# Optimization experiments

Measured on AMD Instinct MI355X. Metric: run time of the kernel, lower is better.

## Reference

```python
import jax, jax.numpy as jnp
import numpy as np
import math

# ---- config (matches init_kwargs / Mamba defaults) ----
B_SZ = 16
IMG = 224
PATCH = 16
D_MODEL = 384
DEPTH = 24
D_INNER = 2 * D_MODEL          # expand=2
D_STATE = 16
D_CONV = 4
DT_RANK = math.ceil(D_MODEL / D_STATE)
N_CLASSES = 1000
L_TOK = (IMG // PATCH) ** 2     # 196

C_CURV = 0.5
SQRT_C = math.sqrt(C_CURV)
MAX_NORM = 0.95 / SQRT_C

# ---- StablePoincareBall ops ----
def _norm(x):
    return jnp.sqrt(jnp.sum(x * x, axis=-1, keepdims=True) + 1e-15)

def expmap0(u):
    n = jnp.clip(_norm(u), 1e-8, 5.0)
    res = jnp.tanh(SQRT_C * n) / SQRT_C * (u / n)
    rn = _norm(res)
    scale = jnp.where(rn > MAX_NORM, MAX_NORM / rn, jnp.ones_like(rn))
    return res * scale

def logmap0(y):
    n = jnp.clip(_norm(y), 1e-8, MAX_NORM)
    return jnp.arctanh(jnp.minimum(SQRT_C * n, 0.95)) / SQRT_C * (y / n)

def mobius_add(a, b):
    xy = jnp.sum(a * b, -1, keepdims=True)
    x2 = jnp.sum(a * a, -1, keepdims=True)
    y2 = jnp.sum(b * b, -1, keepdims=True)
    num = (1 + 2 * C_CURV * xy + C_CURV * y2) * a + (1 - C_CURV * x2) * b
    den = 1 + 2 * C_CURV * xy + (C_CURV ** 2) * x2 * y2
    return num / jnp.maximum(den, 1e-15)

def mobius_matvec(M, x):
    xn = jnp.maximum(_norm(x), 1e-8)
    mx = x @ M.T
    mxn = jnp.maximum(_norm(mx), 1e-8)
    t = jnp.tanh(mxn / xn * jnp.arctanh(jnp.minimum(SQRT_C * xn, 1.0 - 1e-5)))
    return t * mx / (mxn * SQRT_C)

def hyp_layernorm(x, gamma, beta, eps=1e-5):
    t = logmap0(x)
    mean = t.mean(-1, keepdims=True)
    # torch .std() is unbiased (ddof=1)
    var = jnp.sum((t - mean) ** 2, -1, keepdims=True) / (t.shape[-1] - 1)
    tn = (t - mean) / (jnp.sqrt(var) + eps)
    return expmap0(tn * gamma + beta)

def silu(x):
    return x * jax.nn.sigmoid(x)

# ---- Mamba selective scan (recompute dA per step; carry only h) ----
def selective_scan(u, dt, A, Bm, Cm):
    # u, dt: (B,L,Din); A: (Din,N); Bm, Cm: (B,L,N)
    def step(h, inp):
        dt_t, B_t, C_t, u_t = inp              # (B,Din),(B,N),(B,N),(B,Din)
        dA = jnp.exp(dt_t[..., None] * A)      # (B,Din,N)
        h = dA * h + dt_t[..., None] * B_t[:, None, :] * u_t[..., None]
        y = jnp.sum(h * C_t[:, None, :], -1)   # (B,Din)
        return h, y
    h0 = jnp.zeros((u.shape[0], u.shape[2], A.shape[1]), u.dtype)
    _, ys = jax.lax.scan(step, h0, (dt.transpose(1, 0, 2), Bm.transpose(1, 0, 2),
                                    Cm.transpose(1, 0, 2), u.transpose(1, 0, 2)))
    return ys.transpose(1, 0, 2)               # (B,L,Din)

def mamba_mixer(x, in_w, cw, cb, xp_w, dt_w, dt_b, A_log, Dp, out_w):
    xz = x @ in_w.T                            # (B,L,2*Din)
    xc, z = xz[..., :D_INNER], xz[..., D_INNER:]
    xt = xc.transpose(0, 2, 1)                 # (B,Din,L)
    xpad = jnp.pad(xt, ((0, 0), (0, 0), (D_CONV - 1, 0)))
    L = xt.shape[-1]
    conv = sum(cw[:, k][None, :, None] * xpad[:, :, k:k + L] for k in range(D_CONV))
    conv = conv + cb[None, :, None]
    u = silu(conv.transpose(0, 2, 1))          # (B,L,Din)
    dbl = u @ xp_w.T                           # (B,L,dt_rank+2N)
    dt_r = dbl[..., :DT_RANK]
    Bm = dbl[..., DT_RANK:DT_RANK + D_STATE]
    Cm = dbl[..., DT_RANK + D_STATE:]
    dt = jax.nn.softplus(dt_r @ dt_w.T + dt_b)
    A = -jnp.exp(A_log)
    y = selective_scan(u, dt, A, Bm, Cm) + Dp * u
    y = y * silu(z)
    return y @ out_w.T


def setup_inputs() -> dict:
    key = jax.random.key(0)
    ks = jax.random.split(key, 24)
    f32 = jnp.float32
    inp = {}
    inp['x'] = jax.random.normal(ks[0], (B_SZ, 3, IMG, IMG), f32)
    inp['patch_w'] = jax.random.normal(ks[1], (D_MODEL, 3, PATCH, PATCH), f32) * 0.02
    inp['patch_b'] = jax.random.normal(ks[2], (D_MODEL,), f32) * 0.005
    inp['hyp_w'] = jax.random.normal(ks[3], (D_MODEL, D_MODEL), f32) * (1.0 / math.sqrt(D_MODEL))
    inp['hyp_b'] = jax.random.normal(ks[4], (D_MODEL,), f32) * 0.01
    inp['pe_gamma'] = jnp.ones((D_MODEL,), f32)
    inp['pe_beta'] = jnp.zeros((D_MODEL,), f32)
    inp['pos_embed'] = jax.random.normal(ks[5], (1, L_TOK, D_MODEL), f32) * 0.02
    inp['in_proj_w'] = jax.random.normal(ks[6], (DEPTH, 2 * D_INNER, D_MODEL), f32) * 0.02
    inp['conv_w'] = jax.random.normal(ks[7], (DEPTH, D_INNER, D_CONV), f32) * 0.1
    inp['conv_b'] = jnp.zeros((DEPTH, D_INNER), f32)
    inp['x_proj_w'] = jax.random.normal(ks[8], (DEPTH, DT_RANK + 2 * D_STATE, D_INNER), f32) * 0.02
    inp['dt_proj_w'] = jax.random.normal(ks[9], (DEPTH, D_INNER, DT_RANK), f32) * (1.0 / math.sqrt(DT_RANK))
    inp['dt_proj_b'] = jnp.log(jnp.expm1(jnp.full((DEPTH, D_INNER), 0.01, f32)))  # dt init ~0.01
    inp['A_log'] = jnp.tile(jnp.log(jnp.arange(1, D_STATE + 1, dtype=f32))[None, None, :], (DEPTH, D_INNER, 1))
    inp['Dp'] = jnp.ones((DEPTH, D_INNER), f32)
    inp['out_proj_w'] = jax.random.normal(ks[10], (DEPTH, D_MODEL, D_INNER), f32) * (0.02 / math.sqrt(DEPTH))
    inp['gamma'] = jnp.ones((DEPTH, D_MODEL), f32)
    inp['beta'] = jnp.zeros((DEPTH, D_MODEL), f32)
    inp['gamma_f'] = jnp.ones((D_MODEL,), f32)
    inp['beta_f'] = jnp.zeros((D_MODEL,), f32)
    inp['prototypes'] = expmap0(jax.random.normal(ks[11], (N_CLASSES, D_MODEL), f32) * 0.1)
    return inp


def reference(x, patch_w, patch_b, hyp_w, hyp_b, pe_gamma, pe_beta, pos_embed,
              in_proj_w, conv_w, conv_b, x_proj_w, dt_proj_w, dt_proj_b,
              A_log, Dp, out_proj_w, gamma, beta, gamma_f, beta_f, prototypes):
    # patch embed conv
    feat = jax.lax.conv_general_dilated(x, patch_w, (PATCH, PATCH), 'VALID',
                                        dimension_numbers=('NCHW', 'OIHW', 'NCHW'))
    feat = feat + patch_b[None, :, None, None]
    B, D, Hp, Wp = feat.shape
    tokens = feat.reshape(B, D, Hp * Wp).transpose(0, 2, 1)   # (B,L,D)
    h = expmap0(tokens)
    h = mobius_add(mobius_matvec(hyp_w, h), hyp_b)
    h = hyp_layernorm(h, pe_gamma, pe_beta)
    h = expmap0(logmap0(h) + pos_embed)                        # tangent-space pos add
    hidden, residual = h, None
    for i in range(DEPTH):
        residual = hidden if residual is None else hidden + residual
        hn = hyp_layernorm(residual, gamma[i], beta[i])
        hidden = mamba_mixer(hn, in_proj_w[i], conv_w[i], conv_b[i], x_proj_w[i],
                             dt_proj_w[i], dt_proj_b[i], A_log[i], Dp[i], out_proj_w[i])
    residual = hidden + residual
    hf = hyp_layernorm(residual, gamma_f, beta_f)
    pooled = expmap0(logmap0(hf).mean(axis=1))                 # tangent mean pool
    # hyperbolic distance head: logits = -dist(x, prototypes)
    diff = mobius_add(-pooled[:, None, :], prototypes[None])
    dn = jnp.minimum(SQRT_C * _norm(diff)[..., 0], 1.0 - 1e-5)
    return -(2.0 / SQRT_C) * jnp.arctanh(dn)                   # (B, num_classes)
```

## Files before the change

kernel.cpp:

```cpp
#include <hip/hip_runtime.h>
#include <hip/hip_bf16.h>
#include <math.h>

#define D_MODEL 384
#define D_INNER 768
#define D_STATE 16
#define DT_RANK 24
#define NXP 56
#define LTOK 196
#define BSZ 16
#define NROW 3136
#define NDEPTH 24
#define NCLS 1000

constexpr float kSqrtC   = 0.70710678118654752440f;
constexpr float kMaxNorm = 0.95f / 0.70710678118654752440f;

typedef unsigned short u16;
typedef short  bf16x8 __attribute__((ext_vector_type(8)));
typedef u16    u16x8  __attribute__((ext_vector_type(8)));
typedef float  f32x4  __attribute__((ext_vector_type(4)));

__device__ __forceinline__ float clampf(float x, float lo, float hi) {
  return fminf(fmaxf(x, lo), hi);
}

__device__ __forceinline__ u16 f2bf(float f) {
  union { float f; unsigned u; } v; v.f = f;
  return (u16)((v.u + 0x7FFFu + ((v.u >> 16) & 1u)) >> 16);
}
__device__ __forceinline__ float bf2f(u16 s) {
  union { unsigned u; float f; } v; v.u = ((unsigned)s) << 16;
  return v.f;
}

__device__ __forceinline__ void gload16(const u16* g, u16* l) {
  __builtin_amdgcn_global_load_lds(
      (const __attribute__((address_space(1))) unsigned int*)g,
      (__attribute__((address_space(3))) unsigned int*)l, 16, 0, 0);
}

__device__ __forceinline__ float fsig(float x) {
  return __fdividef(1.f, 1.f + __expf(-x));
}
__device__ __forceinline__ float fsilu(float x) { return x * fsig(x); }
__device__ __forceinline__ float fsoftplus(float x) {
  return (x > 20.f) ? x : __logf(1.f + __expf(x));
}
__device__ __forceinline__ float ftanh(float x) {
  float e = __expf(2.f * x);
  return __fdividef(e - 1.f, e + 1.f);
}
__device__ __forceinline__ float fatanh(float x) {
  return 0.5f * __logf(__fdividef(1.f + x, 1.f - x));
}

__device__ __forceinline__ float waveSum(float v) {
#pragma unroll
  for (int o = 1; o < 64; o <<= 1) v += __shfl_xor(v, o, 64);
  return v;
}

__device__ __forceinline__ float blockSum128(float v, float* sm) {
#pragma unroll
  for (int o = 32; o > 0; o >>= 1) v += __shfl_down(v, o, 64);
  __syncthreads();
  if ((threadIdx.x & 63) == 0) sm[threadIdx.x >> 6] = v;
  __syncthreads();
  return sm[0] + sm[1];
}

__global__ __launch_bounds__(256) void k_cvt5(
    const float* __restrict__ s0, u16* __restrict__ d0, int n0,
    const float* __restrict__ s1, u16* __restrict__ d1, int n1,
    const float* __restrict__ s2, u16* __restrict__ d2, int n2,
    const float* __restrict__ s3, u16* __restrict__ d3, int n3,
    const float* __restrict__ s4, u16* __restrict__ d4, int n4) {
  int i = blockIdx.x * 256 + threadIdx.x;
  const float* s; u16* d;
  if (i < n0) { s = s0; d = d0; }
  else if ((i -= n0) < n1) { s = s1; d = d1; }
  else if ((i -= n1) < n2) { s = s2; d = d2; }
  else if ((i -= n2) < n3) { s = s3; d = d3; }
  else if ((i -= n3) < n4) { s = s4; d = d4; }
  else return;
  float4 v = ((const float4*)s)[i];
  short4 o = {(short)f2bf(v.x), (short)f2bf(v.y), (short)f2bf(v.z),
              (short)f2bf(v.w)};
  *(short4*)&d[(size_t)i * 4] = o;
}

__global__ __launch_bounds__(256) void k_im2col(const float* __restrict__ x,
                                                u16* __restrict__ P) {
  size_t idx = (size_t)blockIdx.x * 256 + threadIdx.x;
  if (idx >= (size_t)NROW * 768) return;
  int k = (int)(idx % 768);
  int r = (int)(idx / 768);
  int b = r / LTOK, t = r % LTOK;
  int hp = t / 14, wp = t % 14;
  int c = k / 256, rem = k % 256, i = rem / 16, j = rem % 16;
  P[idx] = f2bf(
      x[(((size_t)(b * 3 + c) * 224) + hp * 16 + i) * 224 + wp * 16 + j]);
}

__global__ __launch_bounds__(256) void k_gemm_bb(
    const u16* __restrict__ A, const u16* __restrict__ W,
    const float* __restrict__ bias, void* __restrict__ Cn,
    void* __restrict__ Ct, int K, int lda, int ldc, int ldct, int Nv, int act,
    int obf, int obf_t) {
  __shared__ u16 As[2][64 * 64];
  __shared__ u16 Ws[2][64 * 64];
  const int tid = threadIdx.x;
  const int m0 = blockIdx.x * 64;
  const int n0 = blockIdx.y * 64;
  const int lane = tid & 63;
  const int w = tid >> 6;
  const int wm = w & 1, wn = w >> 1;
  const int lm = lane & 15;
  const int quad = lane >> 4;
  const int r8 = lane >> 3;
  const int t8 = lane & 7;
  const int gsg = t8 ^ r8;
  const int s = lm & 7;

  f32x4 acc[2][2];
#pragma unroll
  for (int i = 0; i < 2; i++)
#pragma unroll
    for (int j = 0; j < 2; j++) acc[i][j] = (f32x4){0.f, 0.f, 0.f, 0.f};

  const u16* rowA = A + (size_t)(m0 + (2 * w) * 8 + r8) * lda;
  auto stage = [&](int buf, int k0) {
#pragma unroll
    for (int cc = 0; cc < 2; cc++) {
      const int c = 2 * w + cc;
      const int row = c * 8 + r8;
      gload16(A + (size_t)(m0 + row) * lda + k0 + gsg * 8, &As[buf][c * 512]);
      gload16(W + (size_t)(n0 + row) * K + k0 + gsg * 8, &Ws[buf][c * 512]);
    }
  };
  (void)rowA;
  stage(0, 0);
  __syncthreads();
  int cur = 0;
  for (int k0 = 0; k0 < K; k0 += 64) {
    if (k0 + 64 < K) stage(cur ^ 1, k0 + 64);
#pragma unroll
    for (int h = 0; h < 2; h++) {
      const int col = (((h << 2) + quad) ^ s) << 3;
      bf16x8 af[2], bfr[2];
#pragma unroll
      for (int i = 0; i < 2; i++) {
        af[i]  = *(bf16x8*)&As[cur][(wm * 32 + i * 16 + lm) * 64 + col];
        bfr[i] = *(bf16x8*)&Ws[cur][(wn * 32 + i * 16 + lm) * 64 + col];
      }
#pragma unroll
      for (int i = 0; i < 2; i++)
#pragma unroll
        for (int j = 0; j < 2; j++)
          acc[i][j] = __builtin_amdgcn_mfma_f32_16x16x32_bf16(
              af[i], bfr[j], acc[i][j], 0, 0, 0);
    }
    __syncthreads();
    cur ^= 1;
  }
#pragma unroll
  for (int i = 0; i < 2; i++) {
#pragma unroll
    for (int j = 0; j < 2; j++) {
      int cg = n0 + wn * 32 + j * 16 + lm;
      if (cg >= Nv) continue;
      float bj = bias ? bias[cg] : 0.f;
      float o[4];
      int rgb = m0 + wm * 32 + i * 16 + quad * 4;
#pragma unroll
      for (int reg = 0; reg < 4; reg++) {
        float v = acc[i][j][reg] + bj;
        if (act == 1) v = fsoftplus(v);
        else if (act == 2 && cg >= 768) v = fsilu(v);
        o[reg] = v;
      }
      if (Cn) {
#pragma unroll
        for (int reg = 0; reg < 4; reg++) {
          if (obf) ((u16*)Cn)[(size_t)(rgb + reg) * ldc + cg] = f2bf(o[reg]);
          else ((float*)Cn)[(size_t)(rgb + reg) * ldc + cg] = o[reg];
        }
      }
      if (Ct) {
        if (obf_t) {
          short4 o4 = {(short)f2bf(o[0]), (short)f2bf(o[1]), (short)f2bf(o[2]),
                       (short)f2bf(o[3])};
          *(short4*)&((u16*)Ct)[(size_t)cg * ldct + rgb] = o4;
        } else {
          float4 o4 = {o[0], o[1], o[2], o[3]};
          *(float4*)&((float*)Ct)[(size_t)cg * ldct + rgb] = o4;
        }
      }
    }
  }
}

__global__ __launch_bounds__(256) void k_gemm_n128(
    const u16* __restrict__ A, const u16* __restrict__ W,
    const float* __restrict__ bias, void* __restrict__ Cn, int K, int lda,
    int ldc, int act, int obf) {
  __shared__ u16 As[2][64 * 64];
  __shared__ u16 Ws[2][128 * 64];
  const int tid = threadIdx.x;
  const int m0 = blockIdx.x * 64;
  const int n0 = blockIdx.y * 128;
  const int lane = tid & 63;
  const int w = tid >> 6;
  const int lm = lane & 15;
  const int quad = lane >> 4;
  const int r8 = lane >> 3;
  const int t8 = lane & 7;
  const int gsg = t8 ^ r8;
  const int s = lm & 7;

  f32x4 acc[4][2];
#pragma unroll
  for (int i = 0; i < 4; i++)
#pragma unroll
    for (int j = 0; j < 2; j++) acc[i][j] = (f32x4){0.f, 0.f, 0.f, 0.f};

  auto stage = [&](int buf, int k0) {
#pragma unroll
    for (int cc = 0; cc < 2; cc++) {
      const int c = 2 * w + cc;
      gload16(A + (size_t)(m0 + c * 8 + r8) * lda + k0 + gsg * 8,
              &As[buf][c * 512]);
    }
#pragma unroll
    for (int cc = 0; cc < 4; cc++) {
      const int c = 4 * w + cc;
      gload16(W + (size_t)(n0 + c * 8 + r8) * K + k0 + gsg * 8,
              &Ws[buf][c * 512]);
    }
  };
  stage(0, 0);
  __syncthreads();
  int cur = 0;
  for (int k0 = 0; k0 < K; k0 += 64) {
    if (k0 + 64 < K) stage(cur ^ 1, k0 + 64);
#pragma unroll
    for (int h = 0; h < 2; h++) {
      const int col = (((h << 2) + quad) ^ s) << 3;
      bf16x8 af[4], bfr[2];
#pragma unroll
      for (int i = 0; i < 4; i++)
        af[i] = *(bf16x8*)&As[cur][(i * 16 + lm) * 64 + col];
#pragma unroll
      for (int j = 0; j < 2; j++)
        bfr[j] = *(bf16x8*)&Ws[cur][(w * 32 + j * 16 + lm) * 64 + col];
#pragma unroll
      for (int i = 0; i < 4; i++)
#pragma unroll
        for (int j = 0; j < 2; j++)
          acc[i][j] = __builtin_amdgcn_mfma_f32_16x16x32_bf16(
              af[i], bfr[j], acc[i][j], 0, 0, 0);
    }
    __syncthreads();
    cur ^= 1;
  }
#pragma unroll
  for (int i = 0; i < 4; i++) {
#pragma unroll
    for (int j = 0; j < 2; j++) {
      int cg = n0 + w * 32 + j * 16 + lm;
      float bj = bias ? bias[cg] : 0.f;
      int rgb = m0 + i * 16 + quad * 4;
#pragma unroll
      for (int reg = 0; reg < 4; reg++) {
        float v = acc[i][j][reg] + bj;
        if (act == 1) v = fsoftplus(v);
        else if (act == 2 && cg >= 768) v = fsilu(v);
        if (obf) ((u16*)Cn)[(size_t)(rgb + reg) * ldc + cg] = f2bf(v);
        else ((float*)Cn)[(size_t)(rgb + reg) * ldc + cg] = v;
      }
    }
  }
}

__global__ __launch_bounds__(128) void k_stem_a(const float* __restrict__ tok,
                                                u16* __restrict__ hb,
                                                float* __restrict__ xn) {
  __shared__ float sm[2];
  const int r = blockIdx.x, tid = threadIdx.x;
  float v[3];
#pragma unroll
  for (int j = 0; j < 3; j++) v[j] = tok[(size_t)r * D_MODEL + tid + j * 128];
  float s = blockSum128(v[0] * v[0] + v[1] * v[1] + v[2] * v[2], sm);
  float n = sqrtf(s + 1e-15f);
  float nc = clampf(n, 1e-8f, 5.f);
  float ke = tanhf(kSqrtC * nc) / (kSqrtC * nc);
  float rn = sqrtf(ke * ke * s + 1e-15f);
  float sc = rn > kMaxNorm ? kMaxNorm / rn : 1.f;
  float kk = ke * sc;
#pragma unroll
  for (int j = 0; j < 3; j++)
    hb[(size_t)r * D_MODEL + tid + j * 128] = f2bf(kk * v[j]);
  if (tid == 0) xn[r] = fmaxf(sqrtf(kk * kk * s + 1e-15f), 1e-8f);
}

__global__ __launch_bounds__(128) void k_stem_b(
    const float* __restrict__ mx, const float* __restrict__ xn,
    const float* __restrict__ hyp_b, const float* __restrict__ pe_g,
    const float* __restrict__ pe_b, const float* __restrict__ pos,
    float* __restrict__ outh) {
  __shared__ float sm[2];
  const int r = blockIdx.x, tid = threadIdx.x;
  const int t = r % LTOK;
  float mv[3], bv[3];
  int dd[3];
#pragma unroll
  for (int j = 0; j < 3; j++) {
    dd[j] = tid + j * 128;
    mv[j] = mx[(size_t)r * D_MODEL + dd[j]];
    bv[j] = hyp_b[dd[j]];
  }
  float smx = blockSum128(mv[0] * mv[0] + mv[1] * mv[1] + mv[2] * mv[2], sm);
  float mxn = fmaxf(sqrtf(smx + 1e-15f), 1e-8f);
  float xnv = xn[r];
  float tt = tanhf(mxn / xnv * atanhf(fminf(kSqrtC * xnv, 1.f - 1e-5f)));
  float kres = tt / (mxn * kSqrtC);
  float res[3];
#pragma unroll
  for (int j = 0; j < 3; j++) res[j] = kres * mv[j];
  float xy = blockSum128(res[0] * bv[0] + res[1] * bv[1] + res[2] * bv[2], sm);
  float y2 = blockSum128(bv[0] * bv[0] + bv[1] * bv[1] + bv[2] * bv[2], sm);
  float x2 = kres * kres * smx;
  float al = 1.f + xy + 0.5f * y2;
  float be = 1.f - 0.5f * x2;
  float den = fmaxf(1.f + xy + 0.25f * x2 * y2, 1e-15f);
  float h1[3];
#pragma unroll
  for (int j = 0; j < 3; j++) h1[j] = (al * res[j] + be * bv[j]) / den;
  float s1 = blockSum128(h1[0] * h1[0] + h1[1] * h1[1] + h1[2] * h1[2], sm);
  float n1 = sqrtf(s1 + 1e-15f);
  float nc1 = clampf(n1, 1e-8f, kMaxNorm);
  float kl = atanhf(fminf(kSqrtC * nc1, 0.95f)) / (kSqrtC * nc1);
  float tl[3];
#pragma unroll
  for (int j = 0; j < 3; j++) tl[j] = kl * h1[j];
  float mean = blockSum128(tl[0] + tl[1] + tl[2], sm) * (1.f / 384.f);
  float dv = 0.f;
#pragma unroll
  for (int j = 0; j < 3; j++) { float d = tl[j] - mean; dv += d * d; }
  float var = blockSum128(dv, sm) * (1.f / 383.f);
  float inv = 1.f / (sqrtf(var) + 1e-5f);
  float g[3];
#pragma unroll
  for (int j = 0; j < 3; j++)
    g[j] = (tl[j] - mean) * inv * pe_g[dd[j]] + pe_b[dd[j]];
  float sg = blockSum128(g[0] * g[0] + g[1] * g[1] + g[2] * g[2], sm);
  float ng = sqrtf(sg + 1e-15f);
  float nc2 = clampf(ng, 1e-8f, 5.f);
  float ke = tanhf(kSqrtC * nc2) / (kSqrtC * nc2);
  float rn = sqrtf(ke * ke * sg + 1e-15f);
  float sc = rn > kMaxNorm ? kMaxNorm / rn : 1.f;
  float kk = ke * sc;
  float s2 = kk * kk * sg;
  float n3 = sqrtf(s2 + 1e-15f);
  float nc3 = clampf(n3, 1e-8f, kMaxNorm);
  float kl2 = atanhf(fminf(kSqrtC * nc3, 0.95f)) / (kSqrtC * nc3);
  float v[3];
#pragma unroll
  for (int j = 0; j < 3; j++)
    v[j] = kl2 * kk * g[j] + pos[(size_t)t * D_MODEL + dd[j]];
  float sv = blockSum128(v[0] * v[0] + v[1] * v[1] + v[2] * v[2], sm);
  float nv = sqrtf(sv + 1e-15f);
  float nc4 = clampf(nv, 1e-8f, 5.f);
  float ke2 = tanhf(kSqrtC * nc4) / (kSqrtC * nc4);
  float rn2 = sqrtf(ke2 * ke2 * sv + 1e-15f);
  float sc2 = rn2 > kMaxNorm ? kMaxNorm / rn2 : 1.f;
#pragma unroll
  for (int j = 0; j < 3; j++)
    outh[(size_t)r * D_MODEL + dd[j]] = ke2 * sc2 * v[j];
}

__global__ __launch_bounds__(256) void k_resln(
    const float* __restrict__ hid, const float* __restrict__ res_in,
    float* __restrict__ res_out, const float* __restrict__ g_,
    const float* __restrict__ b_, u16* __restrict__ out_bf,
    float* __restrict__ out_f, int first, int out_logmap) {
  const int lane = threadIdx.x & 63;
  const int r = blockIdx.x * 4 + (threadIdx.x >> 6);
  float v[6];
  int dd[6];
#pragma unroll
  for (int j = 0; j < 6; j++) {
    dd[j] = lane + j * 64;
    size_t idx = (size_t)r * D_MODEL + dd[j];
    v[j] = hid[idx] + (first ? 0.f : res_in[idx]);
    res_out[idx] = v[j];
  }
  float ss = 0.f;
#pragma unroll
  for (int j = 0; j < 6; j++) ss += v[j] * v[j];
  float s = waveSum(ss);
  float n = sqrtf(s + 1e-15f);
  float nc = clampf(n, 1e-8f, kMaxNorm);
  float kl = fatanh(fminf(kSqrtC * nc, 0.95f)) / (kSqrtC * nc);
  float t[6];
  float ts = 0.f;
#pragma unroll
  for (int j = 0; j < 6; j++) { t[j] = kl * v[j]; ts += t[j]; }
  float mean = waveSum(ts) * (1.f / 384.f);
  float dv = 0.f;
#pragma unroll
  for (int j = 0; j < 6; j++) { float d = t[j] - mean; dv += d * d; }
  float var = waveSum(dv) * (1.f / 383.f);
  float inv = 1.f / (sqrtf(var) + 1e-5f);
  float g[6];
  float gs = 0.f;
#pragma unroll
  for (int j = 0; j < 6; j++) {
    g[j] = (t[j] - mean) * inv * g_[dd[j]] + b_[dd[j]];
    gs += g[j] * g[j];
  }
  float sg = waveSum(gs);
  float ng = sqrtf(sg + 1e-15f);
  float nc2 = clampf(ng, 1e-8f, 5.f);
  float ke = ftanh(kSqrtC * nc2) / (kSqrtC * nc2);
  float rn = sqrtf(ke * ke * sg + 1e-15f);
  float sc = rn > kMaxNorm ? kMaxNorm / rn : 1.f;
  float kk = ke * sc;
  if (!out_logmap) {
#pragma unroll
    for (int j = 0; j < 6; j++)
      out_bf[(size_t)r * D_MODEL + dd[j]] = f2bf(kk * g[j]);
  } else {
    float s2 = kk * kk * sg;
    float n3 = sqrtf(s2 + 1e-15f);
    float nc3 = clampf(n3, 1e-8f, kMaxNorm);
    float kl2 = fatanh(fminf(kSqrtC * nc3, 0.95f)) / (kSqrtC * nc3);
#pragma unroll
    for (int j = 0; j < 6; j++)
      out_f[(size_t)r * D_MODEL + dd[j]] = kl2 * kk * g[j];
  }
}

__global__ __launch_bounds__(256) void k_convt(const u16* __restrict__ xz,
                                               const float* __restrict__ cw,
                                               const float* __restrict__ cb,
                                               u16* __restrict__ ut,
                                               u16* __restrict__ un) {
  __shared__ u16 sx[52][68];
  __shared__ u16 su2[49][68];
  const int d0 = blockIdx.x * 64;
  const int l0 = blockIdx.y * 49;
  const int b = blockIdx.z;
  const int t = threadIdx.x;
#pragma unroll
  for (int i = 0; i < 4; i++) {
    int idx = t + i * 256;
    if (idx < 832) {
      int row = idx >> 4, seg = idx & 15;
      int l = l0 - 3 + row;
      short4 v = {0, 0, 0, 0};
      if (l >= 0) {
        const u16* p = xz + (size_t)(b * LTOK + l) * (2 * D_INNER) + d0 + seg * 4;
        v = *(const short4*)p;
      }
      *(short4*)&sx[row][seg * 4] = v;
    }
  }
  __syncthreads();
  const int dl = t & 63, lg = t >> 6;
  const int d = d0 + dl;
  const float c0 = cw[d * 4], c1 = cw[d * 4 + 1], c2 = cw[d * 4 + 2],
              c3 = cw[d * 4 + 3];
  const float bb = cb[d];
  for (int l = lg; l < 49; l += 4) {
    float acc = bb;
    acc = fmaf(c0, bf2f(sx[l + 0][dl]), acc);
    acc = fmaf(c1, bf2f(sx[l + 1][dl]), acc);
    acc = fmaf(c2, bf2f(sx[l + 2][dl]), acc);
    acc = fmaf(c3, bf2f(sx[l + 3][dl]), acc);
    su2[l][dl] = f2bf(fsilu(acc));
  }
  __syncthreads();
#pragma unroll
  for (int i = 0; i < 13; i++) {
    int idx = t + i * 256;
    if (idx < 3136) {
      int d_ = idx / 49, l_ = idx % 49;
      ut[(size_t)(d0 + d_) * NROW + b * LTOK + l0 + l_] = su2[l_][d_];
    }
  }
#pragma unroll
  for (int i = 0; i < 13; i++) {
    int idx = t + i * 256;
    if (idx < 3136) {
      int l_ = idx >> 6, d_ = idx & 63;
      un[(size_t)(b * LTOK + l0 + l_) * D_INNER + d0 + d_] = su2[l_][d_];
    }
  }
}

__global__ __launch_bounds__(256) void k_pscan(
    const u16* __restrict__ ut, const float* __restrict__ dblt,
    const float* __restrict__ dt_w, const float* __restrict__ dt_bias,
    const float* __restrict__ A_log, const float* __restrict__ Dp,
    const u16* __restrict__ xz, u16* __restrict__ yf) {
  __shared__ float sdt[4][196];
  __shared__ float su[4][196];
  __shared__ float sprod[16][197];
  const int d0 = blockIdx.x * 4, b = blockIdx.y;
  const int t = threadIdx.x;
  const size_t col0 = (size_t)b * LTOK;
  short4 zq = {0, 0, 0, 0};
  if (t < 196) {
    float r[DT_RANK];
#pragma unroll
    for (int k = 0; k < DT_RANK; k++)
      r[k] = dblt[(size_t)k * NROW + col0 + t];
#pragma unroll
    for (int g = 0; g < 4; g++) {
      const int d = d0 + g;
      float acc = dt_bias[d];
#pragma unroll
      for (int k = 0; k < DT_RANK; k++)
        acc = fmaf(r[k], dt_w[d * DT_RANK + k], acc);
      sdt[g][t] = fsoftplus(acc);
      su[g][t] = bf2f(ut[(size_t)d * NROW + col0 + t]);
    }
    zq = *(const short4*)&xz[(col0 + t) * (2 * D_INNER) + D_INNER + d0];
  }
  const int c = t & 15, n = t >> 4;
  const bool act = c < 14;
  float Breg[14], Creg[14];
  if (act) {
    const float2* Bp =
        (const float2*)(dblt + (size_t)(DT_RANK + n) * NROW + col0 + c * 14);
    const float2* Cp = (const float2*)(
        dblt + (size_t)(DT_RANK + D_STATE + n) * NROW + col0 + c * 14);
#pragma unroll
    for (int j = 0; j < 7; j++) {
      float2 bv = Bp[j], cv = Cp[j];
      Breg[2 * j] = bv.x; Breg[2 * j + 1] = bv.y;
      Creg[2 * j] = cv.x; Creg[2 * j + 1] = cv.y;
    }
  }
  __syncthreads();
  u16 og[4];
  const u16 zz[4] = {(u16)zq.x, (u16)zq.y, (u16)zq.z, (u16)zq.w};
#pragma unroll
  for (int g = 0; g < 4; g++) {
    const int d = d0 + g;
    const float a = -__expf(A_log[(size_t)d * D_STATE + n]);
    float dA[14], hh[14];
    float A = 1.f, Bc = 0.f;
    if (act) {
      float h = 0.f, p = 1.f;
#pragma unroll
      for (int j = 0; j < 14; j++) {
        int l = c * 14 + j;
        float dtv = sdt[g][l];
        float e = __expf(dtv * a);
        h = fmaf(e, h, dtv * Breg[j] * su[g][l]);
        dA[j] = e;
        hh[j] = h;
        p *= e;
      }
      A = p;
      Bc = h;
    }
#pragma unroll
    for (int off = 1; off < 16; off <<= 1) {
      float pA = __shfl_up(A, off, 16);
      float pB = __shfl_up(Bc, off, 16);
      if (c >= off) {
        Bc = fmaf(A, pB, Bc);
        A *= pA;
      }
    }
    float h0 = __shfl_up(Bc, 1, 16);
    if (c == 0) h0 = 0.f;
    if (act) {
      float p = 1.f;
#pragma unroll
      for (int j = 0; j < 14; j++) {
        p *= dA[j];
        sprod[n][c * 14 + j] = fmaf(p, h0, hh[j]) * Creg[j];
      }
    }
    __syncthreads();
    if (t < 196) {
      float y = 0.f;
#pragma unroll
      for (int nn = 0; nn < 16; nn++) y += sprod[nn][t];
      float yv = bf2f(f2bf(fmaf(Dp[d], su[g][t], y)));
      og[g] = f2bf(yv * bf2f(zz[g]));
    }
    __syncthreads();
  }
  if (t < 196) {
    short4 o4 = {(short)og[0], (short)og[1], (short)og[2], (short)og[3]};
    *(short4*)&yf[(col0 + t) * D_INNER + d0] = o4;
  }
}

__global__ __launch_bounds__(128) void k_pool1(const float* __restrict__ tl,
                                               float* __restrict__ partial) {
  const int b = blockIdx.x, g = blockIdx.y, tid = threadIdx.x;
  float m[3] = {0.f, 0.f, 0.f};
  for (int l = g * 14; l < (g + 1) * 14; l++) {
    size_t row = ((size_t)b * LTOK + l) * D_MODEL;
#pragma unroll
    for (int j = 0; j < 3; j++) m[j] += tl[row + tid + j * 128];
  }
#pragma unroll
  for (int j = 0; j < 3; j++)
    partial[((size_t)b * 14 + g) * D_MODEL + tid + j * 128] = m[j];
}

__global__ __launch_bounds__(128) void k_pool2(const float* __restrict__ partial,
                                               float* __restrict__ pooled,
                                               float* __restrict__ x2v) {
  __shared__ float sm[2];
  const int b = blockIdx.x, tid = threadIdx.x;
  float m[3] = {0.f, 0.f, 0.f};
  for (int g = 0; g < 14; g++) {
    size_t row = ((size_t)b * 14 + g) * D_MODEL;
#pragma unroll
    for (int j = 0; j < 3; j++) m[j] += partial[row + tid + j * 128];
  }
#pragma unroll
  for (int j = 0; j < 3; j++) m[j] *= (1.f / (float)LTOK);
  float s = blockSum128(m[0] * m[0] + m[1] * m[1] + m[2] * m[2], sm);
  float n = sqrtf(s + 1e-15f);
  float nc = clampf(n, 1e-8f, 5.f);
  float ke = tanhf(kSqrtC * nc) / (kSqrtC * nc);
  float rn = sqrtf(ke * ke * s + 1e-15f);
  float sc = rn > kMaxNorm ? kMaxNorm / rn : 1.f;
  float kk = ke * sc;
  float p[3];
#pragma unroll
  for (int j = 0; j < 3; j++) {
    p[j] = kk * m[j];
    pooled[(size_t)b * D_MODEL + tid + j * 128] = p[j];
  }
  float s2 = blockSum128(p[0] * p[0] + p[1] * p[1] + p[2] * p[2], sm);
  if (tid == 0) x2v[b] = s2;
}

__global__ __launch_bounds__(256) void k_head(const float* __restrict__ pooled,
                                              const float* __restrict__ protos,
                                              const float* __restrict__ x2v,
                                              float* __restrict__ out) {
  __shared__ float sp[D_MODEL];
  const int b = blockIdx.y;
  const int c = blockIdx.x * 256 + threadIdx.x;
  for (int j = threadIdx.x; j < D_MODEL; j += 256)
    sp[j] = pooled[(size_t)b * D_MODEL + j];
  __syncthreads();
  if (c >= NCLS) return;
  const float* pr = protos + (size_t)c * D_MODEL;
  float dotv = 0.f, y2 = 0.f;
  for (int k = 0; k < D_MODEL; k++) {
    float w = pr[k];
    dotv += sp[k] * w;
    y2 += w * w;
  }
  float x2 = x2v[b];
  float xy = -dotv;
  float al = 1.f + xy + 0.5f * y2;
  float be = 1.f - 0.5f * x2;
  float num2 = al * al * x2 + 2.f * al * be * xy + be * be * y2;
  float den = fmaxf(1.f + xy + 0.25f * x2 * y2, 1e-15f);
  float r2 = num2 / (den * den) + 1e-15f;
  float dn = fminf(kSqrtC * sqrtf(r2), 1.f - 1e-5f);
  out[(size_t)b * NCLS + c] = -(2.f / kSqrtC) * atanhf(dn);
}

extern "C" void kernel_launch(void* const* d_in, const int* in_sizes, int n_in,
                              void* d_out, int out_size, void* d_ws,
                              size_t ws_size, hipStream_t stream) {
  const float* x        = (const float*)d_in[0];
  const float* patch_w  = (const float*)d_in[1];
  const float* patch_b  = (const float*)d_in[2];
  const float* hyp_w    = (const float*)d_in[3];
  const float* hyp_b    = (const float*)d_in[4];
  const float* pe_gamma = (const float*)d_in[5];
  const float* pe_beta  = (const float*)d_in[6];
  const float* pos      = (const float*)d_in[7];
  const float* in_w     = (const float*)d_in[8];
  const float* conv_w   = (const float*)d_in[9];
  const float* conv_b   = (const float*)d_in[10];
  const float* xp_w     = (const float*)d_in[11];
  const float* dt_w     = (const float*)d_in[12];
  const float* dt_bias  = (const float*)d_in[13];
  const float* A_log    = (const float*)d_in[14];
  const float* Dp       = (const float*)d_in[15];
  const float* out_w    = (const float*)d_in[16];
  const float* gamma    = (const float*)d_in[17];
  const float* beta     = (const float*)d_in[18];
  const float* gamma_f  = (const float*)d_in[19];
  const float* beta_f   = (const float*)d_in[20];
  const float* protos   = (const float*)d_in[21];
  float* out = (float*)d_out;

  char* cur = (char*)d_ws;
  auto alloc = [&](size_t bytes) {
    char* p = cur;
    cur += (bytes + 255) & ~(size_t)255;
    return (void*)p;
  };
  float* hidden  = (float*)alloc((size_t)NROW * D_MODEL * 4);
  float* resid   = (float*)alloc((size_t)NROW * D_MODEL * 4);
  float* dblt    = (float*)alloc((size_t)64 * NROW * 4);
  float* fscr    = (float*)alloc((size_t)NROW * 768 * 4);
  float* xn      = (float*)alloc((size_t)NROW * 4);
  float* pooled  = (float*)alloc((size_t)BSZ * D_MODEL * 4);
  float* x2v     = (float*)alloc((size_t)BSZ * 4);
  float* partial = (float*)alloc((size_t)BSZ * 14 * D_MODEL * 4);
  u16* hn_bf  = (u16*)alloc((size_t)NROW * D_MODEL * 2);
  u16* xz_bf  = (u16*)alloc((size_t)NROW * 2 * D_INNER * 2);
  u16* ut     = (u16*)alloc((size_t)D_INNER * NROW * 2);
  u16* u_bf   = (u16*)alloc((size_t)NROW * D_INNER * 2);
  u16* yf     = (u16*)alloc((size_t)NROW * D_INNER * 2);
  const size_t n_inw  = (size_t)NDEPTH * 2 * D_INNER * D_MODEL;
  const size_t n_outw = (size_t)NDEPTH * D_MODEL * D_INNER;
  const size_t n_xpw  = (size_t)NDEPTH * NXP * D_INNER;
  const size_t n_pw   = (size_t)D_MODEL * 768;
  const size_t n_hw   = (size_t)D_MODEL * D_MODEL;
  u16* in_wb  = (u16*)alloc(n_inw * 2);
  u16* out_wb = (u16*)alloc(n_outw * 2);
  u16* xp_wb  = (u16*)alloc(n_xpw * 2);
  u16* p_wb   = (u16*)alloc(n_pw * 2);
  u16* h_wb   = (u16*)alloc(n_hw * 2);
  u16* P_bf     = ut;
  float* tokens = fscr;
  float* mx     = fscr + (size_t)NROW * D_MODEL;
  float* hnf    = fscr;

  {
    const int c0 = (int)(n_inw / 4), c1 = (int)(n_outw / 4),
              c2 = (int)(n_xpw / 4), c3 = (int)(n_pw / 4),
              c4 = (int)(n_hw / 4);
    const int tot = c0 + c1 + c2 + c3 + c4;
    k_cvt5<<<dim3((tot + 255) / 256), dim3(256), 0, stream>>>(
        in_w, in_wb, c0, out_w, out_wb, c1, xp_w, xp_wb, c2, patch_w, p_wb,
        c3, hyp_w, h_wb, c4);
  }

  k_im2col<<<dim3((NROW * 768) / 256), dim3(256), 0, stream>>>(x, P_bf);
  k_gemm_bb<<<dim3(NROW / 64, 6), dim3(256), 0, stream>>>(
      P_bf, p_wb, patch_b, tokens, nullptr, 768, 768, D_MODEL, 0, D_MODEL, 0,
      0, 0);
  k_stem_a<<<dim3(NROW), dim3(128), 0, stream>>>(tokens, hn_bf, xn);
  k_gemm_bb<<<dim3(NROW / 64, 6), dim3(256), 0, stream>>>(
      hn_bf, h_wb, nullptr, mx, nullptr, D_MODEL, D_MODEL, D_MODEL, 0, D_MODEL,
      0, 0, 0);
  k_stem_b<<<dim3(NROW), dim3(128), 0, stream>>>(mx, xn, hyp_b, pe_gamma,
                                                 pe_beta, pos, hidden);
  for (int i = 0; i < NDEPTH; i++) {
    k_resln<<<dim3(NROW / 4), dim3(256), 0, stream>>>(
        hidden, resid, resid, gamma + (size_t)i * D_MODEL,
        beta + (size_t)i * D_MODEL, hn_bf, nullptr, i == 0 ? 1 : 0, 0);
    k_gemm_n128<<<dim3(NROW / 64, (2 * D_INNER) / 128), dim3(256), 0, stream>>>(
        hn_bf, in_wb + (size_t)i * 2 * D_INNER * D_MODEL, nullptr, xz_bf,
        D_MODEL, D_MODEL, 2 * D_INNER, 2, 1);
    k_convt<<<dim3(12, 4, BSZ), dim3(256), 0, stream>>>(
        xz_bf, conv_w + (size_t)i * D_INNER * 4, conv_b + (size_t)i * D_INNER,
        ut, u_bf);
    k_gemm_bb<<<dim3(NROW / 64, 1), dim3(256), 0, stream>>>(
        u_bf, xp_wb + (size_t)i * NXP * D_INNER, nullptr, nullptr, dblt,
        D_INNER, D_INNER, 0, NROW, NXP, 0, 0, 0);
    k_pscan<<<dim3(D_INNER / 4, BSZ), dim3(256), 0, stream>>>(
        ut, dblt, dt_w + (size_t)i * D_INNER * DT_RANK,
        dt_bias + (size_t)i * D_INNER, A_log + (size_t)i * D_INNER * D_STATE,
        Dp + (size_t)i * D_INNER, xz_bf, yf);
    k_gemm_bb<<<dim3(NROW / 64, 6), dim3(256), 0, stream>>>(
        yf, out_wb + (size_t)i * D_MODEL * D_INNER, nullptr, hidden, nullptr,
        D_INNER, D_INNER, D_MODEL, 0, D_MODEL, 0, 0, 0);
  }
  k_resln<<<dim3(NROW / 4), dim3(256), 0, stream>>>(
      hidden, resid, resid, gamma_f, beta_f, nullptr, hnf, 0, 1);
  k_pool1<<<dim3(BSZ, 14), dim3(128), 0, stream>>>(hnf, partial);
  k_pool2<<<dim3(BSZ), dim3(128), 0, stream>>>(partial, pooled, x2v);
  k_head<<<dim3((NCLS + 255) / 256, BSZ), dim3(256), 0, stream>>>(pooled,
                                                                  protos, x2v,
                                                                  out);
}
```

Baseline: 2.169 ms.

## Use 128x128 MFMA GEMM tiles with padded row buffers for projection GEMMs

Replaces the 64x64 and 64x128 GEMM kernels with one 128x128-tile kernel. It uses a 2x2 warp layout where each warp computes a 64x64 subtile. Buffers are padded to 3200 rows so the M dimension divides evenly by 128. The aim is more data reuse per LDS load and fewer redundant global loads. In exchange it raises register and LDS use, lowers occupancy, and launches fewer blocks (e.g. 75 for the out-projection), which may underfill the GPU's compute units. Padded rows read uninitialized memory but only write to padded output regions.

After: 2.383 ms. +9.8%, slower.

```diff
diff --git a/kernel.cpp b/kernel.cpp
--- a/kernel.cpp
+++ b/kernel.cpp
@@ -10,6 +10,7 @@
 #define LTOK 196
 #define BSZ 16
 #define NROW 3136
+#define NROWP 3200
 #define NDEPTH 24
 #define NCLS 1000
 
@@ -129,7 +130,6 @@
 #pragma unroll
     for (int j = 0; j < 2; j++) acc[i][j] = (f32x4){0.f, 0.f, 0.f, 0.f};
 
-  const u16* rowA = A + (size_t)(m0 + (2 * w) * 8 + r8) * lda;
   auto stage = [&](int buf, int k0) {
 #pragma unroll
     for (int cc = 0; cc < 2; cc++) {
@@ -139,7 +139,6 @@
       gload16(W + (size_t)(n0 + row) * K + k0 + gsg * 8, &Ws[buf][c * 512]);
     }
   };
-  (void)rowA;
   stage(0, 0);
   __syncthreads();
   int cur = 0;
@@ -201,17 +200,18 @@
   }
 }
 
-__global__ __launch_bounds__(256) void k_gemm_n128(
+__global__ __launch_bounds__(256) void k_gemm_128(
     const u16* __restrict__ A, const u16* __restrict__ W,
     const float* __restrict__ bias, void* __restrict__ Cn, int K, int lda,
     int ldc, int act, int obf) {
-  __shared__ u16 As[2][64 * 64];
+  __shared__ u16 As[2][128 * 64];
   __shared__ u16 Ws[2][128 * 64];
   const int tid = threadIdx.x;
-  const int m0 = blockIdx.x * 64;
+  const int m0 = blockIdx.x * 128;
   const int n0 = blockIdx.y * 128;
   const int lane = tid & 63;
   const int w = tid >> 6;
+  const int wm = w & 1, wn = w >> 1;
   const int lm = lane & 15;
   const int quad = lane >> 4;
   const int r8 = lane >> 3;
@@ -219,24 +219,19 @@
   const int gsg = t8 ^ r8;
   const int s = lm & 7;
 
-  f32x4 acc[4][2];
+  f32x4 acc[4][4];
 #pragma unroll
   for (int i = 0; i < 4; i++)
 #pragma unroll
-    for (int j = 0; j < 2; j++) acc[i][j] = (f32x4){0.f, 0.f, 0.f, 0.f};
+    for (int j = 0; j < 4; j++) acc[i][j] = (f32x4){0.f, 0.f, 0.f, 0.f};
 
   auto stage = [&](int buf, int k0) {
-#pragma unroll
-    for (int cc = 0; cc < 2; cc++) {
-      const int c = 2 * w + cc;
-      gload16(A + (size_t)(m0 + c * 8 + r8) * lda + k0 + gsg * 8,
-              &As[buf][c * 512]);
-    }
 #pragma unroll
     for (int cc = 0; cc < 4; cc++) {
       const int c = 4 * w + cc;
-      gload16(W + (size_t)(n0 + c * 8 + r8) * K + k0 + gsg * 8,
-              &Ws[buf][c * 512]);
+      const int row = c * 8 + r8;
+      gload16(A + (size_t)(m0 + row) * lda + k0 + gsg * 8, &As[buf][c * 512]);
+      gload16(W + (size_t)(n0 + row) * K + k0 + gsg * 8, &Ws[buf][c * 512]);
     }
   };
   stage(0, 0);
@@ -247,17 +242,16 @@
 #pragma unroll
     for (int h = 0; h < 2; h++) {
       const int col = (((h << 2) + quad) ^ s) << 3;
-      bf16x8 af[4], bfr[2];
+      bf16x8 af[4], bfr[4];
+#pragma unroll
+      for (int i = 0; i < 4; i++) {
+        af[i]  = *(bf16x8*)&As[cur][(wm * 64 + i * 16 + lm) * 64 + col];
+        bfr[i] = *(bf16x8*)&Ws[cur][(wn * 64 + i * 16 + lm) * 64 + col];
+      }
 #pragma unroll
       for (int i = 0; i < 4; i++)
-        af[i] = *(bf16x8*)&As[cur][(i * 16 + lm) * 64 + col];
-#pragma unroll
-      for (int j = 0; j < 2; j++)
-        bfr[j] = *(bf16x8*)&Ws[cur][(w * 32 + j * 16 + lm) * 64 + col];
-#pragma unroll
-      for (int i = 0; i < 4; i++)
-#pragma unroll
-        for (int j = 0; j < 2; j++)
+#pragma unroll
+        for (int j = 0; j < 4; j++)
           acc[i][j] = __builtin_amdgcn_mfma_f32_16x16x32_bf16(
               af[i], bfr[j], acc[i][j], 0, 0, 0);
     }
@@ -267,10 +261,10 @@
 #pragma unroll
   for (int i = 0; i < 4; i++) {
 #pragma unroll
-    for (int j = 0; j < 2; j++) {
-      int cg = n0 + w * 32 + j * 16 + lm;
+    for (int j = 0; j < 4; j++) {
+      int cg = n0 + wn * 64 + j * 16 + lm;
       float bj = bias ? bias[cg] : 0.f;
-      int rgb = m0 + i * 16 + quad * 4;
+      int rgb = m0 + wm * 64 + i * 16 + quad * 4;
 #pragma unroll
       for (int reg = 0; reg < 4; reg++) {
         float v = acc[i][j][reg] + bj;
@@ -709,19 +703,19 @@
     cur += (bytes + 255) & ~(size_t)255;
     return (void*)p;
   };
-  float* hidden  = (float*)alloc((size_t)NROW * D_MODEL * 4);
+  float* hidden  = (float*)alloc((size_t)NROWP * D_MODEL * 4);
   float* resid   = (float*)alloc((size_t)NROW * D_MODEL * 4);
   float* dblt    = (float*)alloc((size_t)64 * NROW * 4);
-  float* fscr    = (float*)alloc((size_t)NROW * 768 * 4);
+  float* fscr    = (float*)alloc((size_t)NROWP * 768 * 4);
   float* xn      = (float*)alloc((size_t)NROW * 4);
   float* pooled  = (float*)alloc((size_t)BSZ * D_MODEL * 4);
   float* x2v     = (float*)alloc((size_t)BSZ * 4);
   float* partial = (float*)alloc((size_t)BSZ * 14 * D_MODEL * 4);
-  u16* hn_bf  = (u16*)alloc((size_t)NROW * D_MODEL * 2);
-  u16* xz_bf  = (u16*)alloc((size_t)NROW * 2 * D_INNER * 2);
-  u16* ut     = (u16*)alloc((size_t)D_INNER * NROW * 2);
+  u16* hn_bf  = (u16*)alloc((size_t)NROWP * D_MODEL * 2);
+  u16* xz_bf  = (u16*)alloc((size_t)NROWP * 2 * D_INNER * 2);
+  u16* ut     = (u16*)alloc((size_t)NROWP * 768 * 2);
   u16* u_bf   = (u16*)alloc((size_t)NROW * D_INNER * 2);
-  u16* yf     = (u16*)alloc((size_t)NROW * D_INNER * 2);
+  u16* yf     = (u16*)alloc((size_t)NROWP * D_INNER * 2);
   const size_t n_inw  = (size_t)NDEPTH * 2 * D_INNER * D_MODEL;
   const size_t n_outw = (size_t)NDEPTH * D_MODEL * D_INNER;
   const size_t n_xpw  = (size_t)NDEPTH * NXP * D_INNER;
@@ -734,7 +728,7 @@
   u16* h_wb   = (u16*)alloc(n_hw * 2);
   u16* P_bf     = ut;
   float* tokens = fscr;
-  float* mx     = fscr + (size_t)NROW * D_MODEL;
+  float* mx     = fscr + (size_t)NROWP * D_MODEL;
   float* hnf    = fscr;
 
   {
@@ -748,22 +742,21 @@
   }
 
   k_im2col<<<dim3((NROW * 768) / 256), dim3(256), 0, stream>>>(x, P_bf);
-  k_gemm_bb<<<dim3(NROW / 64, 6), dim3(256), 0, stream>>>(
-      P_bf, p_wb, patch_b, tokens, nullptr, 768, 768, D_MODEL, 0, D_MODEL, 0,
-      0, 0);
+  k_gemm_128<<<dim3(NROWP / 128, 3), dim3(256), 0, stream>>>(
+      P_bf, p_wb, patch_b, tokens, 768, 768, D_MODEL, 0, 0);
   k_stem_a<<<dim3(NROW), dim3(128), 0, stream>>>(tokens, hn_bf, xn);
-  k_gemm_bb<<<dim3(NROW / 64, 6), dim3(256), 0, stream>>>(
-      hn_bf, h_wb, nullptr, mx, nullptr, D_MODEL, D_MODEL, D_MODEL, 0, D_MODEL,
-      0, 0, 0);
+  k_gemm_128<<<dim3(NROWP / 128, 3), dim3(256), 0, stream>>>(
+      hn_bf, h_wb, nullptr, mx, D_MODEL, D_MODEL, D_MODEL, 0, 0);
   k_stem_b<<<dim3(NROW), dim3(128), 0, stream>>>(mx, xn, hyp_b, pe_gamma,
                                                  pe_beta, pos, hidden);
   for (int i = 0; i < NDEPTH; i++) {
     k_resln<<<dim3(NROW / 4), dim3(256), 0, stream>>>(
         hidden, resid, resid, gamma + (size_t)i * D_MODEL,
         beta + (size_t)i * D_MODEL, hn_bf, nullptr, i == 0 ? 1 : 0, 0);
-    k_gemm_n128<<<dim3(NROW / 64, (2 * D_INNER) / 128), dim3(256), 0, stream>>>(
-        hn_bf, in_wb + (size_t)i * 2 * D_INNER * D_MODEL, nullptr, xz_bf,
-        D_MODEL, D_MODEL, 2 * D_INNER, 2, 1);
+    k_gemm_128<<<dim3(NROWP / 128, (2 * D_INNER) / 128), dim3(256), 0,
+                 stream>>>(hn_bf, in_wb + (size_t)i * 2 * D_INNER * D_MODEL,
+                           nullptr, xz_bf, D_MODEL, D_MODEL, 2 * D_INNER, 2,
+                           1);
     k_convt<<<dim3(12, 4, BSZ), dim3(256), 0, stream>>>(
         xz_bf, conv_w + (size_t)i * D_INNER * 4, conv_b + (size_t)i * D_INNER,
         ut, u_bf);
@@ -774,9 +767,9 @@
         ut, dblt, dt_w + (size_t)i * D_INNER * DT_RANK,
         dt_bias + (size_t)i * D_INNER, A_log + (size_t)i * D_INNER * D_STATE,
         Dp + (size_t)i * D_INNER, xz_bf, yf);
-    k_gemm_bb<<<dim3(NROW / 64, 6), dim3(256), 0, stream>>>(
-        yf, out_wb + (size_t)i * D_MODEL * D_INNER, nullptr, hidden, nullptr,
-        D_INNER, D_INNER, D_MODEL, 0, D_MODEL, 0, 0, 0);
+    k_gemm_128<<<dim3(NROWP / 128, D_MODEL / 128), dim3(256), 0, stream>>>(
+        yf, out_wb + (size_t)i * D_MODEL * D_INNER, nullptr, hidden, D_INNER,
+        D_INNER, D_MODEL, 0, 0);
   }
   k_resln<<<dim3(NROW / 4), dim3(256), 0, stream>>>(
       hidden, resid, resid, gamma_f, beta_f, nullptr, hnf, 0, 1);
```
